# Kernel optimization log

Hardware: AMD Instinct MI355X
Metric: run time of the kernel (lower is better)

Reference implementation:

```python
import jax, jax.numpy as jnp
import numpy as np

EPS = 1e-5

def setup_inputs() -> dict:
    key = jax.random.key(0)
    k1, k2, k3, k4 = jax.random.split(key, 4)
    Cin, Cout, K = 128, 256, 3
    x = jax.random.normal(k1, (32, Cin, 56, 56), dtype=jnp.float32)
    # kaiming_normal fan_in relu: std = sqrt(2 / (Cin*K*K))
    std = np.sqrt(2.0 / (Cin * K * K)).astype(np.float32)
    weight = jax.random.normal(k2, (Cout, Cin, K, K), dtype=jnp.float32) * std
    bias = jnp.zeros((Cout,), dtype=jnp.float32)
    gamma = jnp.ones((Cout,), dtype=jnp.float32)
    beta = jnp.zeros((Cout,), dtype=jnp.float32)
    return {"x": x, "weight": weight, "bias": bias, "gamma": gamma, "beta": beta}

def reference(x, weight, bias, gamma, beta):
    # conv2d, stride=1, padding=1 (NCHW, OIHW)
    y = jax.lax.conv_general_dilated(
        x, weight, window_strides=(1, 1), padding=((1, 1), (1, 1)),
        dimension_numbers=("NCHW", "OIHW", "NCHW"))
    y = y + bias[None, :, None, None]
    # BatchNorm2d, training mode: batch stats over (N,H,W), biased variance
    mean = jnp.mean(y, axis=(0, 2, 3), keepdims=True)
    var = jnp.mean(jnp.square(y - mean), axis=(0, 2, 3), keepdims=True)
    y = (y - mean) * jax.lax.rsqrt(var + EPS)
    y = y * gamma[None, :, None, None] + beta[None, :, None, None]
    return jax.nn.relu(y)
```

## Files before the change

kernel.cpp:

```cpp
#include <hip/hip_runtime.h>
#include <hip/hip_bf16.h>

typedef short v8s __attribute__((ext_vector_type(8)));
typedef float f32x4 __attribute__((ext_vector_type(4)));
typedef unsigned short u16;
typedef unsigned int u32;

#define HW_   3136
#define W_    56
#define PW_   58
#define CIN_  128
#define COUT_ 256
#define NB_   32
#define KCNT  100352.0f

#define XP_ELEMS (NB_*PW_*PW_*CIN_)
#define WT_ELEMS (9*COUT_*CIN_)
#define WT_OFFB  (XP_ELEMS*2)
#define ST_OFFB  (WT_OFFB + WT_ELEMS*2)

#define GLOAD16(g, l) __builtin_amdgcn_global_load_lds( \
    (const __attribute__((address_space(1))) u32*)(g), \
    (__attribute__((address_space(3))) u32*)(l), 16, 0, 0)

extern "C" __global__ void __launch_bounds__(256)
pad_kernel(const float* __restrict__ x, u16* __restrict__ xp)
{
    const int b  = blockIdx.x;
    const int n  = b / PW_;
    const int hp = b % PW_;
    u16* rowp = xp + ((n * PW_ + hp) * PW_) * CIN_;
    const int tid = threadIdx.x;

    if (hp == 0 || hp == PW_ - 1) {
        for (int j = tid; j < PW_ * CIN_ / 8; j += 256)
            *(v8s*)&rowp[j * 8] = (v8s){0,0,0,0,0,0,0,0};
        return;
    }

    __shared__ u16 tile[CIN_ * 57];
    const float* xrow = x + (n * CIN_) * HW_ + (hp - 1) * W_;
    for (int idx = tid; idx < CIN_ * W_; idx += 256) {
        const int c = idx / W_;
        const int w = idx - c * W_;
        __hip_bfloat16 bv = __float2bfloat16(xrow[c * HW_ + w]);
        tile[c * 57 + w] = *(u16*)&bv;
    }
    __syncthreads();

    if (tid < 32) {
        const int wp = (tid >> 4) * (PW_ - 1);
        const int cg = tid & 15;
        *(v8s*)&rowp[wp * CIN_ + cg * 8] = (v8s){0,0,0,0,0,0,0,0};
    }
    for (int idx = tid; idx < W_ * 16; idx += 256) {
        const int wp = (idx >> 4) + 1;
        const int cg = idx & 15;
        v8s v;
        #pragma unroll
        for (int j = 0; j < 8; ++j)
            v[j] = (short)tile[(cg * 8 + j) * 57 + (wp - 1)];
        *(v8s*)&rowp[wp * CIN_ + cg * 8] = v;
    }
}

extern "C" __global__ void wt_kernel(const float* __restrict__ wgt, u16* __restrict__ wt)
{
    const int e   = blockIdx.x * 256 + threadIdx.x;
    const int ci  = e & 127;
    const int t2  = e >> 7;
    const int co  = t2 & 255;
    const int tap = t2 >> 8;
    __hip_bfloat16 b = __float2bfloat16(wgt[co * 1152 + ci * 9 + tap]);
    wt[e] = *(u16*)&b;
}

extern "C" __global__ void __launch_bounds__(256)
conv_kernel(const u16* __restrict__ xp, const u16* __restrict__ wt,
            const float* __restrict__ bias, float* __restrict__ out,
            float* __restrict__ stats)
{
    __shared__ u16 As[128 * 64];
    __shared__ u16 Bs[128 * 64];

    const int t    = threadIdx.x;
    const int lane = t & 63;
    const int wid  = t >> 6;

    const int bid     = blockIdx.x;
    const int logical = (bid & 7) * 196 + (bid >> 3);
    const int cbase   = (logical & 1) << 7;
    const int mbase   = (logical >> 1) << 7;

    const int srow = lane >> 3;
    const int scol = ((lane & 7) ^ srow) << 3;
    int xa[4], wb[4];
    #pragma unroll
    for (int i = 0; i < 4; ++i) {
        const int r   = wid * 32 + i * 8 + srow;
        const int m   = mbase + r;
        const int n0  = m / HW_;
        const int hw0 = m - n0 * HW_;
        const int h0  = hw0 / W_;
        const int w0  = hw0 - h0 * W_;
        xa[i] = ((n0 * PW_ + h0) * PW_ + w0) * CIN_ + scol;
        wb[i] = (cbase + r) * CIN_ + scol;
    }

    f32x4 acc[4][4];
    #pragma unroll
    for (int i = 0; i < 4; ++i)
        #pragma unroll
        for (int j = 0; j < 4; ++j) acc[i][j] = (f32x4){0.f, 0.f, 0.f, 0.f};

    const int wr = wid >> 1, wc = wid & 1;
    const int frow = lane & 15;
    const int kg   = lane >> 4;

    #pragma unroll 1
    for (int kh = 0; kh < 3; ++kh) {
        #pragma unroll 1
        for (int kw = 0; kw < 3; ++kw) {
            const int xoff  = (kh * PW_ + kw) * CIN_;
            const int woff2 = (kh * 3 + kw) * (COUT_ * CIN_);
            #pragma unroll 1
            for (int half = 0; half < 2; ++half) {
                const int cinb = half << 6;
                __syncthreads();
                #pragma unroll
                for (int i = 0; i < 4; ++i) {
                    GLOAD16(xp + xa[i] + xoff + cinb,  &As[(wid * 32 + i * 8) * 64]);
                    GLOAD16(wt + wb[i] + woff2 + cinb, &Bs[(wid * 32 + i * 8) * 64]);
                }
                __syncthreads();
                #pragma unroll
                for (int ks = 0; ks < 2; ++ks) {
                    v8s af[4], bf4[4];
                    #pragma unroll
                    for (int mf = 0; mf < 4; ++mf) {
                        const int row = wr * 64 + mf * 16 + frow;
                        const int ch  = (ks * 4 + kg) ^ (row & 7);
                        af[mf] = *(const v8s*)&As[row * 64 + ch * 8];
                    }
                    #pragma unroll
                    for (int nf = 0; nf < 4; ++nf) {
                        const int row = wc * 64 + nf * 16 + frow;
                        const int ch  = (ks * 4 + kg) ^ (row & 7);
                        bf4[nf] = *(const v8s*)&Bs[row * 64 + ch * 8];
                    }
                    #pragma unroll
                    for (int mf = 0; mf < 4; ++mf)
                        #pragma unroll
                        for (int nf = 0; nf < 4; ++nf)
                            acc[mf][nf] = __builtin_amdgcn_mfma_f32_16x16x32_bf16(
                                af[mf], bf4[nf], acc[mf][nf], 0, 0, 0);
                }
            }
        }
    }

    const int lgrp = lane >> 4;
    #pragma unroll
    for (int nf = 0; nf < 4; ++nf) {
        const int co = cbase + wc * 64 + nf * 16 + frow;
        const float bv = bias[co];
        float s = 0.f, q = 0.f;
        #pragma unroll
        for (int mf = 0; mf < 4; ++mf) {
            const int mloc = wr * 64 + mf * 16 + lgrp * 4;
            const int mg2  = mbase + mloc;
            const int n2   = mg2 / HW_;
            const int hw2  = mg2 - n2 * HW_;
            float4 ov; float vx;
            vx = acc[mf][nf][0] + bv; ov.x = vx; s += vx; q += vx * vx;
            vx = acc[mf][nf][1] + bv; ov.y = vx; s += vx; q += vx * vx;
            vx = acc[mf][nf][2] + bv; ov.z = vx; s += vx; q += vx * vx;
            vx = acc[mf][nf][3] + bv; ov.w = vx; s += vx; q += vx * vx;
            *(float4*)(out + (n2 * COUT_ + co) * HW_ + hw2) = ov;
        }
        s += __shfl_xor(s, 16); s += __shfl_xor(s, 32);
        q += __shfl_xor(q, 16); q += __shfl_xor(q, 32);
        if (lgrp == 0) {
            atomicAdd(&stats[co], s);
            atomicAdd(&stats[COUT_ + co], q);
        }
    }
}

extern "C" __global__ void bn_kernel(float* __restrict__ y, const float* __restrict__ stats,
                                     const float* __restrict__ gamma, const float* __restrict__ beta)
{
    const int i4 = blockIdx.x * 256 + threadIdx.x;
    const int e  = i4 * 4;
    const int co = (e / HW_) & (COUT_ - 1);
    const float inv  = 1.f / KCNT;
    const float mean = stats[co] * inv;
    const float var  = stats[COUT_ + co] * inv - mean * mean;
    const float scale = gamma[co] * rsqrtf(var + 1e-5f);
    const float shift = beta[co] - mean * scale;
    float4 v = *(float4*)(y + e);
    v.x = fmaxf(fmaf(v.x, scale, shift), 0.f);
    v.y = fmaxf(fmaf(v.y, scale, shift), 0.f);
    v.z = fmaxf(fmaf(v.z, scale, shift), 0.f);
    v.w = fmaxf(fmaf(v.w, scale, shift), 0.f);
    *(float4*)(y + e) = v;
}

extern "C" void kernel_launch(void* const* d_in, const int* in_sizes, int n_in,
                              void* d_out, int out_size, void* d_ws, size_t ws_size,
                              hipStream_t stream)
{
    const float* x     = (const float*)d_in[0];
    const float* wgt   = (const float*)d_in[1];
    const float* bias  = (const float*)d_in[2];
    const float* gamma = (const float*)d_in[3];
    const float* beta  = (const float*)d_in[4];
    float* out = (float*)d_out;

    char* ws = (char*)d_ws;
    u16*   xp    = (u16*)ws;
    u16*   wt    = (u16*)(ws + WT_OFFB);
    float* stats = (float*)(ws + ST_OFFB);

    hipMemsetAsync(stats, 0, 2 * COUT_ * sizeof(float), stream);

    pad_kernel<<<NB_ * PW_, 256, 0, stream>>>(x, xp);
    wt_kernel<<<WT_ELEMS / 256, 256, 0, stream>>>(wgt, wt);
    conv_kernel<<<1568, 256, 0, stream>>>(xp, wt, bias, out, stats);
    bn_kernel<<<(out_size / 4) / 256, 256, 0, stream>>>(out, stats, gamma, beta);
}
```

Before: 263.7 us.

## Triple-buffer conv GEMM with 128x256 tiles, 8 waves and interleaved prefetch

The conv kernel moves from a single-buffered 128x128 tile with 4 waves to a 128x256 tile (all output channels) with 8 waves and triple-buffered LDS. Global-to-LDS loads for K-step kt+2 are interleaved with MFMA phases, using explicit vmcnt waits, barriers and setprio to overlap memory with compute. This removes the full sync/load/compute serialization and halves the A-tile reloads across channel halves. The pad kernel also switches to float4 loads with bf16 conversion after the LDS transpose. The cost is more LDS (144KB) and fixed hand-scheduling that is easy to get wrong.

```diff
diff --git a/kernel.cpp b/kernel.cpp
--- a/kernel.cpp
+++ b/kernel.cpp
@@ -28,23 +28,28 @@
 {
     const int b  = blockIdx.x;
     const int n  = b / PW_;
-    const int hp = b % PW_;
-    u16* rowp = xp + ((n * PW_ + hp) * PW_) * CIN_;
+    const int hp = b - n * PW_;
+    u16* rowp = xp + (n * PW_ + hp) * PW_ * CIN_;
     const int tid = threadIdx.x;
 
     if (hp == 0 || hp == PW_ - 1) {
-        for (int j = tid; j < PW_ * CIN_ / 8; j += 256)
-            *(v8s*)&rowp[j * 8] = (v8s){0,0,0,0,0,0,0,0};
+        #pragma unroll
+        for (int k = 0; k < 4; ++k) {
+            const int j = tid + k * 256;
+            if (j < PW_ * CIN_ / 8)
+                *(v8s*)&rowp[j * 8] = (v8s){0,0,0,0,0,0,0,0};
+        }
         return;
     }
 
-    __shared__ u16 tile[CIN_ * 57];
-    const float* xrow = x + (n * CIN_) * HW_ + (hp - 1) * W_;
-    for (int idx = tid; idx < CIN_ * W_; idx += 256) {
-        const int c = idx / W_;
-        const int w = idx - c * W_;
-        __hip_bfloat16 bv = __float2bfloat16(xrow[c * HW_ + w]);
-        tile[c * 57 + w] = *(u16*)&bv;
+    __shared__ float tile[CIN_ * 58];
+    const float* xrow = x + n * CIN_ * HW_ + (hp - 1) * W_;
+    for (int idx = tid; idx < CIN_ * 14; idx += 256) {
+        const int c  = idx / 14;
+        const int w4 = idx - c * 14;
+        const float4 v = *(const float4*)&xrow[c * HW_ + w4 * 4];
+        float* tp = &tile[c * 58 + w4 * 4];
+        tp[0] = v.x; tp[1] = v.y; tp[2] = v.z; tp[3] = v.w;
     }
     __syncthreads();
 
@@ -58,8 +63,10 @@
         const int cg = idx & 15;
         v8s v;
         #pragma unroll
-        for (int j = 0; j < 8; ++j)
-            v[j] = (short)tile[(cg * 8 + j) * 57 + (wp - 1)];
+        for (int j = 0; j < 8; ++j) {
+            __hip_bfloat16 bv = __float2bfloat16(tile[(cg * 8 + j) * 58 + (wp - 1)]);
+            v[j] = *(short*)&bv;
+        }
         *(v8s*)&rowp[wp * CIN_ + cg * 8] = v;
     }
 }
@@ -75,94 +82,174 @@
     wt[e] = *(u16*)&b;
 }
 
-extern "C" __global__ void __launch_bounds__(256)
+#define MFMA4(MF_A, B_, N_) \
+    acc[0][N_] = __builtin_amdgcn_mfma_f32_16x16x32_bf16(a0, B_, acc[0][N_], 0, 0, 0); \
+    acc[1][N_] = __builtin_amdgcn_mfma_f32_16x16x32_bf16(a1, B_, acc[1][N_], 0, 0, 0); \
+    acc[2][N_] = __builtin_amdgcn_mfma_f32_16x16x32_bf16(a2, B_, acc[2][N_], 0, 0, 0); \
+    acc[3][N_] = __builtin_amdgcn_mfma_f32_16x16x32_bf16(a3, B_, acc[3][N_], 0, 0, 0);
+
+#define PHASE_MID() \
+    __builtin_amdgcn_s_barrier(); \
+    asm volatile("s_waitcnt lgkmcnt(0)" ::: "memory"); \
+    __builtin_amdgcn_sched_barrier(0); \
+    __builtin_amdgcn_s_setprio(1);
+
+#define PHASE_END() \
+    __builtin_amdgcn_s_setprio(0); \
+    __builtin_amdgcn_s_barrier();
+
+#define CONV_ITER(KT, C0, C2, VM, PF)                                          \
+{                                                                              \
+    int xoff2 = 0, woff2 = 0;                                                  \
+    if (PF) {                                                                  \
+        const int ktp = (KT) + 2;                                              \
+        const int tap = ktp >> 1;                                              \
+        const int kh  = (tap * 11) >> 5;                                       \
+        const int kw  = tap - kh * 3;                                          \
+        const int cb  = (ktp & 1) << 6;                                        \
+        xoff2 = (kh * PW_ + kw) * CIN_ + cb;                                   \
+        woff2 = tap * (COUT_ * CIN_) + cb;                                     \
+    }                                                                          \
+    const u16* acur = As + (C0) * 8192;                                        \
+    const u16* bcur = Bs + (C0) * 16384;                                       \
+    u16* apre = As + (C2) * 8192;                                              \
+    u16* bpre = Bs + (C2) * 16384;                                             \
+    asm volatile("s_waitcnt vmcnt(" #VM ")" ::: "memory");                     \
+    __builtin_amdgcn_s_barrier();                                              \
+             \
+    if (PF) {                                                                  \
+        GLOAD16(xp + xa0 + xoff2, apre + wid * 512);                           \
+        GLOAD16(xp + xa1 + xoff2, apre + (8 + wid) * 512);                     \
+    }                                                                          \
+    a0 = *(const v8s*)(acur + ar0 + ck0);                                      \
+    a1 = *(const v8s*)(acur + ar1 + ck0);                                      \
+    a2 = *(const v8s*)(acur + ar2 + ck0);                                      \
+    a3 = *(const v8s*)(acur + ar3 + ck0);                                      \
+    b0 = *(const v8s*)(bcur + br0 + ck0);                                      \
+    b1 = *(const v8s*)(bcur + br1 + ck0);                                      \
+    PHASE_MID();                                                               \
+    MFMA4(a, b0, 0); MFMA4(a, b1, 1);                                          \
+    PHASE_END();                                                               \
+                 \
+    if (PF) {                                                                  \
+        GLOAD16(wt + wb0 + woff2, bpre + wid * 512);                           \
+        GLOAD16(wt + wb1 + woff2, bpre + (8 + wid) * 512);                     \
+    }                                                                          \
+    b2 = *(const v8s*)(bcur + br2 + ck0);                                      \
+    b3 = *(const v8s*)(bcur + br3 + ck0);                                      \
+    PHASE_MID();                                                               \
+    MFMA4(a, b2, 2); MFMA4(a, b3, 3);                                          \
+    PHASE_END();                                                               \
+         \
+    if (PF) {                                                                  \
+        GLOAD16(wt + wb2 + woff2, bpre + (16 + wid) * 512);                    \
+        GLOAD16(wt + wb3 + woff2, bpre + (24 + wid) * 512);                    \
+    }                                                                          \
+    a0 = *(const v8s*)(acur + ar0 + ck1);                                      \
+    a1 = *(const v8s*)(acur + ar1 + ck1);                                      \
+    a2 = *(const v8s*)(acur + ar2 + ck1);                                      \
+    a3 = *(const v8s*)(acur + ar3 + ck1);                                      \
+    b0 = *(const v8s*)(bcur + br0 + ck1);                                      \
+    b1 = *(const v8s*)(bcur + br1 + ck1);                                      \
+    PHASE_MID();                                                               \
+    MFMA4(a, b0, 0); MFMA4(a, b1, 1);                                          \
+    PHASE_END();                                                               \
+                                  \
+    b2 = *(const v8s*)(bcur + br2 + ck1);                                      \
+    b3 = *(const v8s*)(bcur + br3 + ck1);                                      \
+    PHASE_MID();                                                               \
+    MFMA4(a, b2, 2); MFMA4(a, b3, 3);                                          \
+    PHASE_END();                                                               \
+}
+
+extern "C" __global__ void __launch_bounds__(512)
 conv_kernel(const u16* __restrict__ xp, const u16* __restrict__ wt,
             const float* __restrict__ bias, float* __restrict__ out,
             float* __restrict__ stats)
 {
-    __shared__ u16 As[128 * 64];
-    __shared__ u16 Bs[128 * 64];
+    __shared__ u16 As[3 * 128 * 64];
+    __shared__ u16 Bs[3 * 256 * 64];
 
     const int t    = threadIdx.x;
     const int lane = t & 63;
     const int wid  = t >> 6;
 
-    const int bid     = blockIdx.x;
-    const int logical = (bid & 7) * 196 + (bid >> 3);
-    const int cbase   = (logical & 1) << 7;
-    const int mbase   = (logical >> 1) << 7;
-
-    const int srow = lane >> 3;
-    const int scol = ((lane & 7) ^ srow) << 3;
-    int xa[4], wb[4];
-    #pragma unroll
-    for (int i = 0; i < 4; ++i) {
-        const int r   = wid * 32 + i * 8 + srow;
-        const int m   = mbase + r;
-        const int n0  = m / HW_;
-        const int hw0 = m - n0 * HW_;
-        const int h0  = hw0 / W_;
-        const int w0  = hw0 - h0 * W_;
-        xa[i] = ((n0 * PW_ + h0) * PW_ + w0) * CIN_ + scol;
-        wb[i] = (cbase + r) * CIN_ + scol;
-    }
+    const int bid   = blockIdx.x;
+    const int mbase = ((bid & 7) * 98 + (bid >> 3)) << 7;
+
+    const int srow8 = lane >> 3;
+    const int swz   = ((lane & 7) ^ srow8) << 3;
+    int xa0, xa1, wb0, wb1, wb2, wb3;
+    {
+        #pragma unroll
+        for (int j = 0; j < 2; ++j) {
+            const int r  = (j * 8 + wid) * 8 + srow8;
+            const int m  = mbase + r;
+            const int n0 = m / HW_;
+            const int hw0 = m - n0 * HW_;
+            const int h0 = hw0 / W_;
+            const int w0 = hw0 - h0 * W_;
+            const int a  = ((n0 * PW_ + h0) * PW_ + w0) * CIN_ + swz;
+            if (j == 0) xa0 = a; else xa1 = a;
+        }
+        #pragma unroll
+        for (int i = 0; i < 4; ++i) {
+            const int r = (i * 8 + wid) * 8 + srow8;
+            const int a = r * CIN_ + swz;
+            if (i == 0) wb0 = a; else if (i == 1) wb1 = a;
+            else if (i == 2) wb2 = a; else wb3 = a;
+        }
+    }
+
+    const int wr = wid >> 2, wc = wid & 3;
+    const int frow = lane & 15;
+    const int kg   = lane >> 4;
+    const int ck0  = ((kg)     ^ (frow & 7)) << 3;
+    const int ck1  = ((4 | kg) ^ (frow & 7)) << 3;
+    const int ar0 = (wr * 64 +  0 + frow) * 64;
+    const int ar1 = (wr * 64 + 16 + frow) * 64;
+    const int ar2 = (wr * 64 + 32 + frow) * 64;
+    const int ar3 = (wr * 64 + 48 + frow) * 64;
+    const int br0 = (wc * 64 +  0 + frow) * 64;
+    const int br1 = (wc * 64 + 16 + frow) * 64;
+    const int br2 = (wc * 64 + 32 + frow) * 64;
+    const int br3 = (wc * 64 + 48 + frow) * 64;
 
     f32x4 acc[4][4];
     #pragma unroll
     for (int i = 0; i < 4; ++i)
         #pragma unroll
         for (int j = 0; j < 4; ++j) acc[i][j] = (f32x4){0.f, 0.f, 0.f, 0.f};
-
-    const int wr = wid >> 1, wc = wid & 1;
-    const int frow = lane & 15;
-    const int kg   = lane >> 4;
+    v8s a0, a1, a2, a3, b0, b1, b2, b3;
+
+    GLOAD16(xp + xa0,      As + wid * 512);
+    GLOAD16(xp + xa1,      As + (8 + wid) * 512);
+    GLOAD16(wt + wb0,      Bs + wid * 512);
+    GLOAD16(wt + wb1,      Bs + (8 + wid) * 512);
+    GLOAD16(wt + wb2,      Bs + (16 + wid) * 512);
+    GLOAD16(wt + wb3,      Bs + (24 + wid) * 512);
+    GLOAD16(xp + xa0 + 64, As + 8192  + wid * 512);
+    GLOAD16(xp + xa1 + 64, As + 8192  + (8 + wid) * 512);
+    GLOAD16(wt + wb0 + 64, Bs + 16384 + wid * 512);
+    GLOAD16(wt + wb1 + 64, Bs + 16384 + (8 + wid) * 512);
+    GLOAD16(wt + wb2 + 64, Bs + 16384 + (16 + wid) * 512);
+    GLOAD16(wt + wb3 + 64, Bs + 16384 + (24 + wid) * 512);
 
     #pragma unroll 1
-    for (int kh = 0; kh < 3; ++kh) {
-        #pragma unroll 1
-        for (int kw = 0; kw < 3; ++kw) {
-            const int xoff  = (kh * PW_ + kw) * CIN_;
-            const int woff2 = (kh * 3 + kw) * (COUT_ * CIN_);
-            #pragma unroll 1
-            for (int half = 0; half < 2; ++half) {
-                const int cinb = half << 6;
-                __syncthreads();
-                #pragma unroll
-                for (int i = 0; i < 4; ++i) {
-                    GLOAD16(xp + xa[i] + xoff + cinb,  &As[(wid * 32 + i * 8) * 64]);
-                    GLOAD16(wt + wb[i] + woff2 + cinb, &Bs[(wid * 32 + i * 8) * 64]);
-                }
-                __syncthreads();
-                #pragma unroll
-                for (int ks = 0; ks < 2; ++ks) {
-                    v8s af[4], bf4[4];
-                    #pragma unroll
-                    for (int mf = 0; mf < 4; ++mf) {
-                        const int row = wr * 64 + mf * 16 + frow;
-                        const int ch  = (ks * 4 + kg) ^ (row & 7);
-                        af[mf] = *(const v8s*)&As[row * 64 + ch * 8];
-                    }
-                    #pragma unroll
-                    for (int nf = 0; nf < 4; ++nf) {
-                        const int row = wc * 64 + nf * 16 + frow;
-                        const int ch  = (ks * 4 + kg) ^ (row & 7);
-                        bf4[nf] = *(const v8s*)&Bs[row * 64 + ch * 8];
-                    }
-                    #pragma unroll
-                    for (int mf = 0; mf < 4; ++mf)
-                        #pragma unroll
-                        for (int nf = 0; nf < 4; ++nf)
-                            acc[mf][nf] = __builtin_amdgcn_mfma_f32_16x16x32_bf16(
-                                af[mf], bf4[nf], acc[mf][nf], 0, 0, 0);
-                }
-            }
-        }
-    }
+    for (int g = 0; g < 5; ++g) {
+        const int kt = g * 3;
+        CONV_ITER(kt,     0, 2, 6, 1);
+        CONV_ITER(kt + 1, 1, 0, 6, 1);
+        CONV_ITER(kt + 2, 2, 1, 6, 1);
+    }
+    CONV_ITER(15, 0, 2, 6, 1);
+    CONV_ITER(16, 1, 0, 6, 0);
+    CONV_ITER(17, 2, 1, 0, 0);
 
     const int lgrp = lane >> 4;
     #pragma unroll
     for (int nf = 0; nf < 4; ++nf) {
-        const int co = cbase + wc * 64 + nf * 16 + frow;
+        const int co = wc * 64 + nf * 16 + frow;
         const float bv = bias[co];
         float s = 0.f, q = 0.f;
         #pragma unroll
@@ -226,6 +313,6 @@
 
     pad_kernel<<<NB_ * PW_, 256, 0, stream>>>(x, xp);
     wt_kernel<<<WT_ELEMS / 256, 256, 0, stream>>>(wgt, wt);
-    conv_kernel<<<1568, 256, 0, stream>>>(xp, wt, bias, out, stats);
+    conv_kernel<<<784, 512, 0, stream>>>(xp, wt, bias, out, stats);
     bn_kernel<<<(out_size / 4) / 256, 256, 0, stream>>>(out, stats, gamma, beta);
 }
```

After: 295.1 us. 11.9% more time.

## Double-buffer conv LDS tiles and merge preprocessing kernels into one launch

Applied to the files above, without the earlier changes.

The conv main loop now uses two LDS buffers per operand, so the global-to-LDS loads for the next K-tile are issued before the MFMAs on the current tile, with a single barrier per iteration. The pad, weight-transpose and stats-zeroing steps are fused into one pre_kernel launch, which removes the memset and one kernel launch. The pad path also loads x with float4 reads into a float tile and converts to bf16 when writing out. Doubling LDS to 64KB per block may reduce occupancy. The new code relies on the global_load_lds writes being complete at the barrier that ends each iteration.

```diff
diff --git a/kernel.cpp b/kernel.cpp
--- a/kernel.cpp
+++ b/kernel.cpp
@@ -19,32 +19,57 @@
 #define WT_OFFB  (XP_ELEMS*2)
 #define ST_OFFB  (WT_OFFB + WT_ELEMS*2)
 
+#define PAD_BLOCKS (NB_*PW_)
+#define WT_BLOCKS  (WT_ELEMS/256)
+
 #define GLOAD16(g, l) __builtin_amdgcn_global_load_lds( \
     (const __attribute__((address_space(1))) u32*)(g), \
     (__attribute__((address_space(3))) u32*)(l), 16, 0, 0)
 
 extern "C" __global__ void __launch_bounds__(256)
-pad_kernel(const float* __restrict__ x, u16* __restrict__ xp)
-{
-    const int b  = blockIdx.x;
+pre_kernel(const float* __restrict__ x, const float* __restrict__ wgt,
+           u16* __restrict__ xp, u16* __restrict__ wt, float* __restrict__ stats)
+{
+    const int b   = blockIdx.x;
+    const int tid = threadIdx.x;
+
+    if (b >= PAD_BLOCKS) {
+        const int e   = (b - PAD_BLOCKS) * 256 + tid;
+        const int ci  = e & 127;
+        const int t2  = e >> 7;
+        const int co  = t2 & 255;
+        const int tap = t2 >> 8;
+        __hip_bfloat16 bv = __float2bfloat16(wgt[co * 1152 + ci * 9 + tap]);
+        wt[e] = *(u16*)&bv;
+        if (b == PAD_BLOCKS) {
+            stats[tid] = 0.f;
+            stats[tid + 256] = 0.f;
+        }
+        return;
+    }
+
     const int n  = b / PW_;
-    const int hp = b % PW_;
-    u16* rowp = xp + ((n * PW_ + hp) * PW_) * CIN_;
-    const int tid = threadIdx.x;
+    const int hp = b - n * PW_;
+    u16* rowp = xp + (n * PW_ + hp) * PW_ * CIN_;
 
     if (hp == 0 || hp == PW_ - 1) {
-        for (int j = tid; j < PW_ * CIN_ / 8; j += 256)
-            *(v8s*)&rowp[j * 8] = (v8s){0,0,0,0,0,0,0,0};
+        #pragma unroll
+        for (int k = 0; k < 4; ++k) {
+            const int j = tid + k * 256;
+            if (j < PW_ * CIN_ / 8)
+                *(v8s*)&rowp[j * 8] = (v8s){0,0,0,0,0,0,0,0};
+        }
         return;
     }
 
-    __shared__ u16 tile[CIN_ * 57];
-    const float* xrow = x + (n * CIN_) * HW_ + (hp - 1) * W_;
-    for (int idx = tid; idx < CIN_ * W_; idx += 256) {
-        const int c = idx / W_;
-        const int w = idx - c * W_;
-        __hip_bfloat16 bv = __float2bfloat16(xrow[c * HW_ + w]);
-        tile[c * 57 + w] = *(u16*)&bv;
+    __shared__ float tile[CIN_ * 58];
+    const float* xrow = x + n * CIN_ * HW_ + (hp - 1) * W_;
+    for (int idx = tid; idx < CIN_ * 14; idx += 256) {
+        const int c  = idx / 14;
+        const int w4 = idx - c * 14;
+        const float4 v = *(const float4*)&xrow[c * HW_ + w4 * 4];
+        float* tp = &tile[c * 58 + w4 * 4];
+        tp[0] = v.x; tp[1] = v.y; tp[2] = v.z; tp[3] = v.w;
     }
     __syncthreads();
 
@@ -58,21 +83,12 @@
         const int cg = idx & 15;
         v8s v;
         #pragma unroll
-        for (int j = 0; j < 8; ++j)
-            v[j] = (short)tile[(cg * 8 + j) * 57 + (wp - 1)];
+        for (int j = 0; j < 8; ++j) {
+            __hip_bfloat16 bv = __float2bfloat16(tile[(cg * 8 + j) * 58 + (wp - 1)]);
+            v[j] = *(short*)&bv;
+        }
         *(v8s*)&rowp[wp * CIN_ + cg * 8] = v;
     }
-}
-
-extern "C" __global__ void wt_kernel(const float* __restrict__ wgt, u16* __restrict__ wt)
-{
-    const int e   = blockIdx.x * 256 + threadIdx.x;
-    const int ci  = e & 127;
-    const int t2  = e >> 7;
-    const int co  = t2 & 255;
-    const int tap = t2 >> 8;
-    __hip_bfloat16 b = __float2bfloat16(wgt[co * 1152 + ci * 9 + tap]);
-    wt[e] = *(u16*)&b;
 }
 
 extern "C" __global__ void __launch_bounds__(256)
@@ -80,8 +96,8 @@
             const float* __restrict__ bias, float* __restrict__ out,
             float* __restrict__ stats)
 {
-    __shared__ u16 As[128 * 64];
-    __shared__ u16 Bs[128 * 64];
+    __shared__ u16 As[2 * 128 * 64];
+    __shared__ u16 Bs[2 * 128 * 64];
 
     const int t    = threadIdx.x;
     const int lane = t & 63;
@@ -92,19 +108,19 @@
     const int cbase   = (logical & 1) << 7;
     const int mbase   = (logical >> 1) << 7;
 
-    const int srow = lane >> 3;
-    const int scol = ((lane & 7) ^ srow) << 3;
+    const int srow8 = lane >> 3;
+    const int swz   = ((lane & 7) ^ srow8) << 3;
     int xa[4], wb[4];
     #pragma unroll
     for (int i = 0; i < 4; ++i) {
-        const int r   = wid * 32 + i * 8 + srow;
+        const int r   = wid * 32 + i * 8 + srow8;
         const int m   = mbase + r;
         const int n0  = m / HW_;
         const int hw0 = m - n0 * HW_;
         const int h0  = hw0 / W_;
         const int w0  = hw0 - h0 * W_;
-        xa[i] = ((n0 * PW_ + h0) * PW_ + w0) * CIN_ + scol;
-        wb[i] = (cbase + r) * CIN_ + scol;
+        xa[i] = ((n0 * PW_ + h0) * PW_ + w0) * CIN_ + swz;
+        wb[i] = (cbase + r) * CIN_ + swz;
     }
 
     f32x4 acc[4][4];
@@ -117,46 +133,54 @@
     const int frow = lane & 15;
     const int kg   = lane >> 4;
 
+    #pragma unroll
+    for (int i = 0; i < 4; ++i) {
+        GLOAD16(xp + xa[i], As + (wid * 32 + i * 8) * 64);
+        GLOAD16(wt + wb[i], Bs + (wid * 32 + i * 8) * 64);
+    }
+    __syncthreads();
+
     #pragma unroll 1
-    for (int kh = 0; kh < 3; ++kh) {
-        #pragma unroll 1
-        for (int kw = 0; kw < 3; ++kw) {
-            const int xoff  = (kh * PW_ + kw) * CIN_;
-            const int woff2 = (kh * 3 + kw) * (COUT_ * CIN_);
-            #pragma unroll 1
-            for (int half = 0; half < 2; ++half) {
-                const int cinb = half << 6;
-                __syncthreads();
+    for (int kt = 0; kt < 18; ++kt) {
+        const int cur = kt & 1;
+        const u16* acur = As + cur * 8192;
+        const u16* bcur = Bs + cur * 8192;
+
+        if (kt < 17) {
+            const int ktn  = kt + 1;
+            const int tap  = ktn >> 1;
+            const int kh   = (tap * 11) >> 5;
+            const int kw   = tap - kh * 3;
+            const int xoff = (kh * PW_ + kw) * CIN_ + ((ktn & 1) << 6);
+            const int woff = tap * (COUT_ * CIN_) + ((ktn & 1) << 6);
+            u16* apre = As + (cur ^ 1) * 8192;
+            u16* bpre = Bs + (cur ^ 1) * 8192;
+            #pragma unroll
+            for (int i = 0; i < 4; ++i) {
+                GLOAD16(xp + xa[i] + xoff, apre + (wid * 32 + i * 8) * 64);
+                GLOAD16(wt + wb[i] + woff, bpre + (wid * 32 + i * 8) * 64);
+            }
+        }
+
+        #pragma unroll
+        for (int ks = 0; ks < 2; ++ks) {
+            const int ck = (((ks << 2) | kg) ^ (frow & 7)) << 3;
+            v8s af[4], bf4[4];
+            #pragma unroll
+            for (int mf = 0; mf < 4; ++mf)
+                af[mf] = *(const v8s*)(acur + (wr * 64 + mf * 16 + frow) * 64 + ck);
+            #pragma unroll
+            for (int nf = 0; nf < 4; ++nf)
+                bf4[nf] = *(const v8s*)(bcur + (wc * 64 + nf * 16 + frow) * 64 + ck);
+            #pragma unroll
+            for (int mf = 0; mf < 4; ++mf)
                 #pragma unroll
-                for (int i = 0; i < 4; ++i) {
-                    GLOAD16(xp + xa[i] + xoff + cinb,  &As[(wid * 32 + i * 8) * 64]);
-                    GLOAD16(wt + wb[i] + woff2 + cinb, &Bs[(wid * 32 + i * 8) * 64]);
-                }
-                __syncthreads();
-                #pragma unroll
-                for (int ks = 0; ks < 2; ++ks) {
-                    v8s af[4], bf4[4];
-                    #pragma unroll
-                    for (int mf = 0; mf < 4; ++mf) {
-                        const int row = wr * 64 + mf * 16 + frow;
-                        const int ch  = (ks * 4 + kg) ^ (row & 7);
-                        af[mf] = *(const v8s*)&As[row * 64 + ch * 8];
-                    }
-                    #pragma unroll
-                    for (int nf = 0; nf < 4; ++nf) {
-                        const int row = wc * 64 + nf * 16 + frow;
-                        const int ch  = (ks * 4 + kg) ^ (row & 7);
-                        bf4[nf] = *(const v8s*)&Bs[row * 64 + ch * 8];
-                    }
-                    #pragma unroll
-                    for (int mf = 0; mf < 4; ++mf)
-                        #pragma unroll
-                        for (int nf = 0; nf < 4; ++nf)
-                            acc[mf][nf] = __builtin_amdgcn_mfma_f32_16x16x32_bf16(
-                                af[mf], bf4[nf], acc[mf][nf], 0, 0, 0);
-                }
-            }
-        }
+                for (int nf = 0; nf < 4; ++nf)
+                    acc[mf][nf] = __builtin_amdgcn_mfma_f32_16x16x32_bf16(
+                        af[mf], bf4[nf], acc[mf][nf], 0, 0, 0);
+        }
+
+        __syncthreads();
     }
 
     const int lgrp = lane >> 4;
@@ -222,10 +246,7 @@
     u16*   wt    = (u16*)(ws + WT_OFFB);
     float* stats = (float*)(ws + ST_OFFB);
 
-    hipMemsetAsync(stats, 0, 2 * COUT_ * sizeof(float), stream);
-
-    pad_kernel<<<NB_ * PW_, 256, 0, stream>>>(x, xp);
-    wt_kernel<<<WT_ELEMS / 256, 256, 0, stream>>>(wgt, wt);
+    pre_kernel<<<PAD_BLOCKS + WT_BLOCKS, 256, 0, stream>>>(x, wgt, xp, wt, stats);
     conv_kernel<<<1568, 256, 0, stream>>>(xp, wt, bias, out, stats);
     bn_kernel<<<(out_size / 4) / 256, 256, 0, stream>>>(out, stats, gamma, beta);
 }
```

Result: slower. 273.7 us (+3.8%).
